# Kernel optimization log

Hardware: AMD Instinct MI355X
Metric: run time of the kernel (lower is better)

Reference implementation:

```python
import jax, jax.numpy as jnp
import numpy as np
import math

B, S, HID = 1, 2048, 4096
NH, NKV, HD = 32, 8, 128
N_REP = NH // NKV
ROPE_THETA = 10000.0


def setup_inputs() -> dict:
    key = jax.random.key(0)
    ks = jax.random.split(key, 5)
    hidden_states = jax.random.normal(ks[0], (B, S, HID), dtype=jnp.float32)
    # additive causal mask: 0 on/below diagonal, -1e9 above
    causal = jnp.triu(jnp.full((S, S), -1e9, dtype=jnp.float32), k=1)
    attention_mask = causal[None, None, :, :]
    wq = jax.random.normal(ks[1], (HID, NH * HD), dtype=jnp.float32) * 0.02
    wk = jax.random.normal(ks[2], (HID, NKV * HD), dtype=jnp.float32) * 0.02
    wv = jax.random.normal(ks[3], (HID, NKV * HD), dtype=jnp.float32) * 0.02
    wo = jax.random.normal(ks[4], (NH * HD, HID), dtype=jnp.float32) * 0.02
    return {"hidden_states": hidden_states, "attention_mask": attention_mask,
            "wq": wq, "wk": wk, "wv": wv, "wo": wo}


def _rope_cos_sin(seq_len, head_dim, base, dtype):
    inv_freq = 1.0 / (base ** (jnp.arange(0, head_dim, 2, dtype=jnp.float32) / head_dim))
    t = jnp.arange(seq_len, dtype=jnp.float32)
    freqs = jnp.outer(t, inv_freq)          # [S, HD/2]
    emb = jnp.concatenate([freqs, freqs], axis=-1)  # [S, HD]
    return jnp.cos(emb).astype(dtype), jnp.sin(emb).astype(dtype)


def _rotate_interleaved(x):
    # pairs (x0,x1) -> (-x1, x0), interleaved (matches torch stack/reshape trick)
    xp = x.reshape(*x.shape[:-1], -1, 2)
    return jnp.stack([-xp[..., 1], xp[..., 0]], axis=-1).reshape(x.shape)


def reference(hidden_states, attention_mask, wq, wk, wv, wo):
    b, s, _ = hidden_states.shape
    q = (hidden_states @ wq).reshape(b, s, NH, HD).transpose(0, 2, 1, 3)   # [B,NH,S,HD]
    k = (hidden_states @ wk).reshape(b, s, NKV, HD).transpose(0, 2, 1, 3)  # [B,NKV,S,HD]
    v = (hidden_states @ wv).reshape(b, s, NKV, HD).transpose(0, 2, 1, 3)

    cos, sin = _rope_cos_sin(s, HD, ROPE_THETA, hidden_states.dtype)
    cos = cos[None, None, :, :]  # broadcast over batch and heads
    sin = sin[None, None, :, :]
    q = q * cos + _rotate_interleaved(q) * sin
    k = k * cos + _rotate_interleaved(k) * sin

    # repeat_kv: [B,NKV,S,HD] -> [B,NH,S,HD]
    k = jnp.repeat(k, N_REP, axis=1)
    v = jnp.repeat(v, N_REP, axis=1)

    scores = jnp.einsum('bhqd,bhkd->bhqk', q, k) / math.sqrt(HD)
    scores = scores + attention_mask
    attn = jax.nn.softmax(scores.astype(jnp.float32), axis=-1).astype(q.dtype)
    out = jnp.einsum('bhqk,bhkd->bhqd', attn, v)          # [B,NH,S,HD]
    out = out.transpose(0, 2, 1, 3).reshape(b, s, NH * HD)
    return out @ wo
```

## Files before the change

kernel.cpp:

```cpp
#include <hip/hip_runtime.h>

#define S_LEN 2048
#define HID 4096
#define NH 32
#define NKV 8
#define HD 128
#define KVW 1024
#define NQKV 6144

typedef _Float16 f16;
typedef _Float16 f16x8 __attribute__((ext_vector_type(8)));
typedef _Float16 f16x4 __attribute__((ext_vector_type(4)));
typedef float f32x4 __attribute__((ext_vector_type(4)));
typedef float f32x16 __attribute__((ext_vector_type(16)));
typedef unsigned int u32;
typedef u32 u32x4 __attribute__((ext_vector_type(4)));

__device__ __forceinline__ void gll16(const void* g, void* lds) {
  __builtin_amdgcn_global_load_lds((const __attribute__((address_space(1))) void*)g,
                                   (__attribute__((address_space(3))) void*)lds, 16, 0, 0);
}

template<int N> __device__ __forceinline__ void vmwait() {
  if constexpr (N == 0) asm volatile("s_waitcnt vmcnt(0)" ::: "memory");
  else if constexpr (N == 2) asm volatile("s_waitcnt vmcnt(2)" ::: "memory");
  else if constexpr (N == 3) asm volatile("s_waitcnt vmcnt(3)" ::: "memory");
  else if constexpr (N == 4) asm volatile("s_waitcnt vmcnt(4)" ::: "memory");
  else if constexpr (N == 5) asm volatile("s_waitcnt vmcnt(5)" ::: "memory");
  else if constexpr (N == 6) asm volatile("s_waitcnt vmcnt(6)" ::: "memory");
  else if constexpr (N == 7) asm volatile("s_waitcnt vmcnt(7)" ::: "memory");
  else if constexpr (N == 8) asm volatile("s_waitcnt vmcnt(8)" ::: "memory");
  else static_assert(N == 0, "add vmcnt case");
}
#define LGKM0 asm volatile("s_waitcnt lgkmcnt(0)" ::: "memory")
#define BAR() __builtin_amdgcn_s_barrier()

__global__ __launch_bounds__(256) void k_prep(
    const float* __restrict__ hs, const float* __restrict__ wq,
    const float* __restrict__ wk, const float* __restrict__ wv,
    const float* __restrict__ wo,
    f16* __restrict__ Hh, f16* __restrict__ Wt, f16* __restrict__ Wot,
    float4* __restrict__ trig)
{
  __shared__ float tile[32][33];
  int bid = blockIdx.x;
  int t = threadIdx.x;
  if (bid >= 40960) {
    int b2 = bid - 40960;
    if (b2 < 4096) {
      size_t i = ((size_t)b2 * 256 + t) * 8;
      float4 a = *(const float4*)(hs + i);
      float4 b = *(const float4*)(hs + i + 4);
      f16x8 o = { (f16)a.x, (f16)a.y, (f16)a.z, (f16)a.w,
                  (f16)b.x, (f16)b.y, (f16)b.z, (f16)b.w };
      *(f16x8*)(Hh + i) = o;
    } else {
      int id = (b2 - 4096) * 256 + t;
      int s = id >> 6, i = id & 63;
      float f0 = powf(10000.f, -(float)((2 * i) & 63) / 64.f);
      float f1 = powf(10000.f, -(float)((2 * i + 1) & 63) / 64.f);
      float a0 = (float)s * f0, a1 = (float)s * f1;
      trig[id] = make_float4(cosf(a0), cosf(a1), sinf(a0), sinf(a1));
    }
    return;
  }
  const float* src; f16* dst; int N; int r;
  if (bid < 16384)      { src = wq; dst = Wt;                          N = 4096; r = bid; }
  else if (bid < 20480) { src = wk; dst = Wt + (size_t)4096 * 4096;    N = 1024; r = bid - 16384; }
  else if (bid < 24576) { src = wv; dst = Wt + (size_t)5120 * 4096;    N = 1024; r = bid - 20480; }
  else                  { src = wo; dst = Wot;                         N = 4096; r = bid - 24576; }
  int tpr = N >> 5;
  int kb = (r / tpr) * 32, nb = (r % tpr) * 32;
  {
    int kl = t >> 3, ng = t & 7;
    float4 v = *(const float4*)(src + (size_t)(kb + kl) * N + nb + ng * 4);
    tile[kl][ng * 4 + 0] = v.x; tile[kl][ng * 4 + 1] = v.y;
    tile[kl][ng * 4 + 2] = v.z; tile[kl][ng * 4 + 3] = v.w;
  }
  __syncthreads();
  {
    int nl = t >> 3, kg = t & 7;
    f16x4 o = { (f16)tile[kg * 4 + 0][nl], (f16)tile[kg * 4 + 1][nl],
                (f16)tile[kg * 4 + 2][nl], (f16)tile[kg * 4 + 3][nl] };
    *(f16x4*)(dst + (size_t)(nb + nl) * HID + kb + kg * 4) = o;
  }
}

extern __shared__ char smem[];

__global__ __launch_bounds__(512, 2) void k_gemm8(
    const f16* __restrict__ A, const f16* __restrict__ Bt,
    f16* __restrict__ Qr, f16* __restrict__ Kr, f16* __restrict__ Vt,
    const float4* __restrict__ trig)
{
  constexpr int BN = 192;
  constexpr int NF = 3;
  constexpr int BCALLS = BN / 64;
  constexpr int BBYTES = BN * 128;
  constexpr int TI = 4 + BCALLS;
  constexpr int W_END = TI, W_MID = TI + 1;
  constexpr int NT = 64;

  const int tid = threadIdx.x, ln = tid & 63, w = tid >> 6;
  const int la = ln & 15, lg = ln >> 4;
  const int wr = w >> 2, wc = w & 3;

  int bx, by;
  {
    int b = blockIdx.y * gridDim.x + blockIdx.x;
    int cx = gridDim.x >> 3;
    int xcd = b & 7, rr = b >> 3;
    bx = xcd * cx + (rr % cx);
    by = rr / cx;
  }
  const int m0 = by * 256, n0 = bx * BN;

  const char* asrcA[2];
#pragma unroll
  for (int c = 0; c < 2; ++c) {
    int row = c * 128 + (tid >> 2);
    int sg = (tid & 3) ^ ((row >> 1) & 3);
    asrcA[c] = (const char*)A + ((size_t)(m0 + row) * HID) * 2 + (size_t)sg * 16;
  }
  const char* bsrcB[BCALLS];
#pragma unroll
  for (int c = 0; c < BCALLS; ++c) {
    int row = c * 64 + (tid >> 3);
    int g = (tid & 7) ^ (row & 7);
    bsrcB[c] = (const char*)Bt + ((size_t)(n0 + row) * HID) * 2 + (size_t)g * 16;
  }
  char* const Bbase = smem + 65536;
  const int d16 = tid * 16;

  auto stA = [&](int t, int h) {
    char* b = smem + (((2 * t + h) & 3) * 16384) + d16;
    size_t off = (size_t)t * 128 + h * 64;
    gll16(asrcA[0] + off, b); gll16(asrcA[1] + off, b + 8192);
  };
  auto stB = [&](int t, int c) {
    char* b = Bbase + (t % 3) * BBYTES + c * 8192 + d16;
    gll16(bsrcB[c] + (size_t)t * 128, b);
  };
  f16x8 af[4], bf[NF];
  auto ldA = [&](int t, int mh, int ks) {
    const char* sb = smem + (((2 * t + ks) & 3) * 16384);
#pragma unroll
    for (int i = 0; i < 4; ++i) {
      int rl = wr * 128 + mh * 64 + i * 16 + la;
      af[i] = *(const f16x8*)(sb + rl * 64 + ((lg ^ ((rl >> 1) & 3)) * 16));
    }
  };
  auto ldB = [&](int t, int ks) {
    const char* sb = Bbase + (t % 3) * BBYTES;
#pragma unroll
    for (int n = 0; n < NF; ++n) {
      int rb = wc * (NF * 16) + n * 16 + la;
      bf[n] = *(const f16x8*)(sb + rb * 128 + (((ks * 4 + lg) ^ (rb & 7)) * 16));
    }
  };

  f32x4 acc[8][NF] = {};

#define MM12(MH)                                                                      \
  __builtin_amdgcn_s_setprio(1);                                                      \
  _Pragma("unroll")                                                                   \
  for (int i = 0; i < 4; ++i)                                                         \
    _Pragma("unroll")                                                                 \
    for (int n = 0; n < NF; ++n)                                                      \
      acc[(MH)*4 + i][n] =                                                            \
        __builtin_amdgcn_mfma_f32_16x16x32_f16(af[i], bf[n], acc[(MH)*4 + i][n], 0, 0, 0); \
  __builtin_amdgcn_s_setprio(0);

  stA(0, 0); stA(0, 1);
  for (int c = 0; c < BCALLS; ++c) stB(0, c);
  stA(1, 0);
  for (int c = 0; c < BCALLS; ++c) stB(1, c);
  vmwait<BCALLS + 2>();
  BAR();

  for (int t = 0; t < NT; ++t) {
    ldA(t, 0, 0); ldB(t, 0);
    if (t + 1 < NT) stA(t + 1, 1);
    BAR(); LGKM0;
    MM12(0);
    BAR();
    ldA(t, 1, 0);
    if (t + 2 < NT) stB(t + 2, 0);
    BAR(); LGKM0;
    MM12(1);
    if (t < NT - 2) vmwait<W_MID>(); else vmwait<0>();
    BAR();
    ldA(t, 0, 1); ldB(t, 1);
    if (t + 2 < NT) { stA(t + 2, 0); stB(t + 2, 1); }
    BAR(); LGKM0;
    MM12(0);
    BAR();
    ldA(t, 1, 1);
    if (t + 2 < NT) stB(t + 2, 2);
    BAR(); LGKM0;
    MM12(1);
    if (t < NT - 2) vmwait<W_END>(); else vmwait<0>();
    BAR();
  }
#undef MM12

#pragma unroll
  for (int mi = 0; mi < 8; ++mi) {
#pragma unroll
    for (int nf = 0; nf < NF; ++nf) {
      f32x4 fr = acc[mi][nf];
      int n = n0 + wc * (NF * 16) + nf * 16 + la;
      int mr = m0 + wr * 128 + mi * 16 + lg * 4;
      if (n < HID + KVW) {
        int d = n & 127;
#pragma unroll
        for (int r = 0; r < 4; ++r) {
          float v = fr[r];
          float p = __shfl_xor(v, 1);
          float4 tc = trig[(size_t)(mr + r) * 64 + (d >> 1)];
          float cv = (d & 1) ? tc.y : tc.x;
          float sv = (d & 1) ? tc.w : tc.z;
          float o = v * cv + ((d & 1) ? p : -p) * sv;
          if (n < HID) Qr[(size_t)(mr + r) * HID + n] = (f16)o;
          else         Kr[(size_t)(mr + r) * KVW + (n - HID)] = (f16)o;
        }
      } else {
        int nv = n - (HID + KVW);
        f16x4 o4 = { (f16)fr[0], (f16)fr[1], (f16)fr[2], (f16)fr[3] };
        *(f16x4*)(Vt + (size_t)nv * S_LEN + mr) = o4;
      }
    }
  }
}

template<int MODE, int MF, int NF, int WM, int WN>
__global__ __launch_bounds__(WM * WN * 64, 2) void k_gemm4(
    const f16* __restrict__ A, const f16* __restrict__ Bt,
    f16* __restrict__ Qr, f16* __restrict__ Kr, f16* __restrict__ Vt,
    const float4* __restrict__ trig, float* __restrict__ Cout)
{
  constexpr int NTHR = WM * WN * 64;
  constexpr int BM = WM * MF * 16;
  constexpr int BN = WN * NF * 16;
  constexpr int ABYTES = BM * 128;
  constexpr int BBYTES = BN * 128;
  constexpr int RPC = NTHR / 8;
  constexpr int ACALLS = BM / RPC;
  constexpr int BCALLS = BN / RPC;
  constexpr int NT = 64;

  const int tid = threadIdx.x, ln = tid & 63, w = tid >> 6;
  const int la = ln & 15, lg = ln >> 4;
  const int wr = w / WN, wc = w % WN;

  int bx, by;
  {
    int b = blockIdx.y * gridDim.x + blockIdx.x;
    int cx = gridDim.x >> 3;
    int xcd = b & 7, rr = b >> 3;
    bx = xcd * cx + (rr % cx);
    by = rr / cx;
  }
  const int m0 = by * BM, n0 = bx * BN;

  const char* asrc[ACALLS];
  const char* bsrc[BCALLS];
  int adst[ACALLS > BCALLS ? ACALLS : BCALLS];
#pragma unroll
  for (int c = 0; c < ACALLS; ++c) {
    int r = c * RPC + (tid >> 3);
    int g = (tid & 7) ^ (r & 7);
    asrc[c] = (const char*)A + ((size_t)(m0 + r) * HID + (size_t)g * 8) * 2;
    adst[c] = c * NTHR * 16 + tid * 16;
  }
#pragma unroll
  for (int c = 0; c < BCALLS; ++c) {
    int r = c * RPC + (tid >> 3);
    int g = (tid & 7) ^ (r & 7);
    bsrc[c] = (const char*)Bt + ((size_t)(n0 + (r >= BN ? r - BN : r)) * HID + (size_t)g * 8) * 2;
  }

  char* const Bbase = smem + 2 * ABYTES;
  f32x4 acc[MF][NF] = {};

#pragma unroll
  for (int c = 0; c < ACALLS; ++c) gll16(asrc[c], smem + adst[c]);
#pragma unroll
  for (int c = 0; c < BCALLS; ++c) gll16(bsrc[c], Bbase + adst[c]);
#pragma unroll
  for (int c = 0; c < BCALLS; ++c) gll16(bsrc[c] + 128, Bbase + 1 * BBYTES + adst[c]);
#pragma unroll
  for (int c = 0; c < BCALLS; ++c) gll16(bsrc[c] + 256, Bbase + 2 * BBYTES + adst[c]);
  vmwait<2 * BCALLS>();
  __builtin_amdgcn_s_barrier();

  for (int t = 0; t < NT; ++t) {
    if (t + 1 < NT) {
      char* sa = smem + ((t + 1) & 1) * ABYTES;
#pragma unroll
      for (int c = 0; c < ACALLS; ++c) gll16(asrc[c] + (size_t)(t + 1) * 128, sa + adst[c]);
    }
    if (t + 3 < NT) {
      char* sb = Bbase + ((t + 3) & 3) * BBYTES;
#pragma unroll
      for (int c = 0; c < BCALLS; ++c) gll16(bsrc[c] + (size_t)(t + 3) * 128, sb + adst[c]);
    }
    const char* sa = smem + (t & 1) * ABYTES;
    const char* sb = Bbase + (t & 3) * BBYTES;
#pragma unroll
    for (int ks = 0; ks < 2; ++ks) {
      f16x8 af[MF], bf[NF];
#pragma unroll
      for (int i = 0; i < MF; ++i) {
        int rl = wr * MF * 16 + i * 16 + la;
        af[i] = *(const f16x8*)(sa + rl * 128 + (((ks * 4 + lg) ^ (rl & 7)) * 16));
      }
#pragma unroll
      for (int n = 0; n < NF; ++n) {
        int rb = wc * NF * 16 + n * 16 + la;
        bf[n] = *(const f16x8*)(sb + rb * 128 + (((ks * 4 + lg) ^ (rb & 7)) * 16));
      }
      __builtin_amdgcn_s_setprio(1);
#pragma unroll
      for (int i = 0; i < MF; ++i)
#pragma unroll
        for (int n = 0; n < NF; ++n)
          acc[i][n] = __builtin_amdgcn_mfma_f32_16x16x32_f16(af[i], bf[n], acc[i][n], 0, 0, 0);
      __builtin_amdgcn_s_setprio(0);
    }
    if (t < NT - 3)      vmwait<BCALLS>();
    else if (t < NT - 1) vmwait<0>();
    if (t < NT - 1) __builtin_amdgcn_s_barrier();
  }

#pragma unroll
  for (int mi = 0; mi < MF; ++mi) {
#pragma unroll
    for (int nf = 0; nf < NF; ++nf) {
      f32x4 fr = acc[mi][nf];
      int n = n0 + wc * NF * 16 + nf * 16 + la;
      int mr = m0 + wr * MF * 16 + mi * 16 + lg * 4;
      if (MODE == 1) {
#pragma unroll
        for (int r = 0; r < 4; ++r)
          Cout[(size_t)(mr + r) * HID + n] = fr[r];
      }
    }
  }
}

#define KBYTES (64 * 128 * 2)
#define VBYTES (128 * 64 * 2)

__global__ __launch_bounds__(256, 2) void k_attn(
    const f16* __restrict__ Qr, const f16* __restrict__ Kr, const f16* __restrict__ Vt,
    f16* __restrict__ AO)
{
  int bid = blockIdx.x;
  int h, c;
  if (bid < 256) { h = bid >> 3; c = bid & 7; }
  else           { int t = bid - 256; h = t >> 3; c = 15 - (t & 7); }
  const int hkv = h >> 2;
  const int q0c = c * 128;
  const int NT = 2 * c + 2;

  __shared__ char KV[2][KBYTES + VBYTES];

  const int tid = threadIdx.x;
  const int ln = tid & 63, w = tid >> 6;
  const int q = ln & 31;
  const int hi = ln >> 5;
  const int qg = q0c + w * 32 + q;

  size_t ksrc[4], vsrc[4];
  int kdo[4], vdo[4];
#pragma unroll
  for (int j = 0; j < 4; ++j) {
    int kc = w * 4 + j;
    int kr = kc * 4 + (ln >> 4);
    ksrc[j] = ((size_t)kr * KVW + hkv * HD) * 2 + (size_t)(((ln & 15) ^ (kr & 7)) * 16);
    kdo[j] = kc * 1024;
    int vc = w * 4 + j;
    int d = vc * 8 + (ln >> 3);
    vsrc[j] = ((size_t)(hkv * HD + d) * S_LEN) * 2 + (size_t)(((ln & 7) ^ (d & 7)) * 16);
    vdo[j] = KBYTES + vc * 1024;
  }

  f16x8 qf[8];
  {
    const f16* qrow = Qr + (size_t)qg * HID + h * HD + hi * 8;
#pragma unroll
    for (int ks = 0; ks < 8; ++ks) qf[ks] = *(const f16x8*)(qrow + ks * 16);
  }

  f32x16 ot[4] = {};
  float m2 = -3.0e38f, l = 0.f;
  const float K2 = 0.12753256471f;

  int buf = 0;
#pragma unroll
  for (int j = 0; j < 4; ++j) {
    gll16((const char*)Kr + ksrc[j], &KV[0][kdo[j]]);
    gll16((const char*)Vt + vsrc[j], &KV[0][vdo[j]]);
  }

  for (int jt = 0; jt < NT; ++jt) {
    __syncthreads();
    if (jt + 1 < NT) {
      size_t ko = (size_t)(jt + 1) * 64 * KVW * 2;
      size_t vo = (size_t)(jt + 1) * 64 * 2;
#pragma unroll
      for (int j = 0; j < 4; ++j) {
        gll16((const char*)Kr + ksrc[j] + ko, &KV[buf ^ 1][kdo[j]]);
        gll16((const char*)Vt + vsrc[j] + vo, &KV[buf ^ 1][vdo[j]]);
      }
    }
    const int j0 = jt * 64;
    if (j0 <= q0c + w * 32 + 31) {
      const f16* Kb = (const f16*)&KV[buf][0];
      const f16* Vb = (const f16*)&KV[buf][KBYTES];
      f32x16 s0 = {}, s1 = {};
#pragma unroll
      for (int ks = 0; ks < 8; ++ks) {
        int cc = ((ks * 2 + hi) ^ (q & 7)) * 8;
        f16x8 k0 = *(const f16x8*)(Kb + q * 128 + cc);
        f16x8 k1 = *(const f16x8*)(Kb + (q + 32) * 128 + cc);
        s0 = __builtin_amdgcn_mfma_f32_32x32x16_f16(k0, qf[ks], s0, 0, 0, 0);
        s1 = __builtin_amdgcn_mfma_f32_32x32x16_f16(k1, qf[ks], s1, 0, 0, 0);
      }
      const bool nm = (j0 + 63 > q0c + w * 32);
      float p0[16], p1[16];
      float mx = -3.0e38f;
#pragma unroll
      for (int r = 0; r < 16; ++r) {
        float a = s0[r], b = s1[r];
        if (nm) {
          int kvb = j0 + (r & 3) + 8 * (r >> 2) + 4 * hi;
          if (kvb > qg) a = -3.0e38f;
          if (kvb + 32 > qg) b = -3.0e38f;
        }
        p0[r] = a; p1[r] = b;
        mx = fmaxf(mx, fmaxf(a, b));
      }
      mx = fmaxf(mx, __shfl_xor(mx, 32));
      float m2c = mx * K2;
      int defer = (m2c <= m2 + 11.0f);
      if (!__all(defer)) {
        float m2n = fmaxf(m2, m2c);
        float corr = exp2f(m2 - m2n);
        m2 = m2n; l *= corr;
#pragma unroll
        for (int t = 0; t < 4; ++t)
#pragma unroll
          for (int r = 0; r < 16; ++r) ot[t][r] *= corr;
      }
      float sum = 0.f;
#pragma unroll
      for (int r = 0; r < 16; ++r) {
        p0[r] = exp2f(__builtin_fmaf(p0[r], K2, -m2));
        p1[r] = exp2f(__builtin_fmaf(p1[r], K2, -m2));
        sum += p0[r] + p1[r];
      }
      l += sum + __shfl_xor(sum, 32);
      u32 pw0[8], pw1[8];
#pragma unroll
      for (int t = 0; t < 8; ++t) {
        pw0[t] = __builtin_bit_cast(u32, __builtin_amdgcn_cvt_pkrtz(p0[2 * t], p0[2 * t + 1]));
        pw1[t] = __builtin_bit_cast(u32, __builtin_amdgcn_cvt_pkrtz(p1[2 * t], p1[2 * t + 1]));
      }
      f16x8 pf[4];
#pragma unroll
      for (int ch = 0; ch < 2; ++ch) {
        const u32* pw = ch ? pw1 : pw0;
        u32 sx[8];
#pragma unroll
        for (int t = 0; t < 8; ++t) sx[t] = (u32)__shfl_xor((int)pw[t], 32);
        u32x4 fa = { hi ? sx[2] : pw[0], hi ? sx[3] : pw[1],
                     hi ? pw[2] : sx[0], hi ? pw[3] : sx[1] };
        u32x4 fb = { hi ? sx[6] : pw[4], hi ? sx[7] : pw[5],
                     hi ? pw[6] : sx[4], hi ? pw[7] : sx[5] };
        pf[ch * 2 + 0] = __builtin_bit_cast(f16x8, fa);
        pf[ch * 2 + 1] = __builtin_bit_cast(f16x8, fb);
      }
#pragma unroll
      for (int dt = 0; dt < 4; ++dt) {
        int d = dt * 32 + q;
#pragma unroll
        for (int f = 0; f < 4; ++f) {
          f16x8 vf = *(const f16x8*)(Vb + d * 64 + (((f * 2 + hi) ^ (q & 7)) * 8));
          ot[dt] = __builtin_amdgcn_mfma_f32_32x32x16_f16(vf, pf[f], ot[dt], 0, 0, 0);
        }
      }
    }
    buf ^= 1;
  }

  __syncthreads();
  char* scr = &KV[0][0] + w * 8192;
  float inv = 1.f / l;
#pragma unroll
  for (int dt = 0; dt < 4; ++dt) {
#pragma unroll
    for (int rg = 0; rg < 4; ++rg) {
      u32 wa = __builtin_bit_cast(u32, __builtin_amdgcn_cvt_pkrtz(ot[dt][rg * 4 + 0] * inv, ot[dt][rg * 4 + 1] * inv));
      u32 wb = __builtin_bit_cast(u32, __builtin_amdgcn_cvt_pkrtz(ot[dt][rg * 4 + 2] * inv, ot[dt][rg * 4 + 3] * inv));
      int byte = q * 256 + (((dt * 4 + rg) ^ (q & 7)) * 16) + hi * 8;
      u32* p = (u32*)(scr + byte);
      p[0] = wa; p[1] = wb;
    }
  }
  asm volatile("s_waitcnt lgkmcnt(0)" ::: "memory");
#pragma unroll
  for (int ps = 0; ps < 8; ++ps) {
    int qr = ps * 4 + (ln >> 4);
    int ck = (ln & 15) ^ (qr & 7);
    f16x8 v = *(const f16x8*)(scr + qr * 256 + ck * 16);
    *(f16x8*)(AO + (size_t)(q0c + w * 32 + qr) * HID + h * HD + (ln & 15) * 8) = v;
  }
}

extern "C" void kernel_launch(void* const* d_in, const int* in_sizes, int n_in,
                              void* d_out, int out_size, void* d_ws, size_t ws_size,
                              hipStream_t stream) {
  const float* hs = (const float*)d_in[0];
  const float* wq = (const float*)d_in[2];
  const float* wk = (const float*)d_in[3];
  const float* wv = (const float*)d_in[4];
  const float* wo = (const float*)d_in[5];
  float* out = (float*)d_out;

  char* ws = (char*)d_ws;
  size_t off = 0;
  auto alloc = [&](size_t b) { char* p = ws + off; off += (b + 255) & ~(size_t)255; return p; };
  f16* Hh   = (f16*)alloc((size_t)S_LEN * HID * 2);
  f16* Wt   = (f16*)alloc((size_t)NQKV * HID * 2);
  float4* trig = (float4*)alloc((size_t)S_LEN * 64 * sizeof(float4));
  f16* Qrp  = (f16*)alloc((size_t)S_LEN * HID * 2);
  f16* Krp  = (f16*)alloc((size_t)S_LEN * KVW * 2);
  f16* Vtp  = (f16*)alloc((size_t)KVW * S_LEN * 2);
  f16* AO   = (f16*)alloc((size_t)S_LEN * HID * 2);
  f16* Wot  = (f16*)alloc((size_t)HID * HID * 2);

  hipFuncSetAttribute((const void*)k_gemm8,
                      hipFuncAttributeMaxDynamicSharedMemorySize, 139264);
  hipFuncSetAttribute((const void*)k_gemm4<1, 8, 2, 2, 4>,
                      hipFuncAttributeMaxDynamicSharedMemorySize, 131072);

  k_prep<<<45568, 256, 0, stream>>>(hs, wq, wk, wv, wo, Hh, Wt, Wot, trig);
  k_gemm8<<<dim3(NQKV / 192, S_LEN / 256), 512, 139264, stream>>>(
      Hh, Wt, Qrp, Krp, Vtp, trig);
  k_attn<<<dim3(512), 256, 0, stream>>>(Qrp, Krp, Vtp, AO);
  k_gemm4<1, 8, 2, 2, 4><<<dim3(HID / 128, S_LEN / 256), 512, 131072, stream>>>(
      AO, Wot, nullptr, nullptr, nullptr, nullptr, out);
}
```

Baseline: 323.4 us.

## Reuse gemm8 pipeline for output projection and widen prep transpose tiles

The output projection GEMM now uses the templated k_gemm8 kernel, with BN=128 and a plain fp32 store epilogue, in place of the separate k_gemm4 kernel. That swaps in the finer-grained A/B staging schedule the QKV GEMM already uses. The weight transpose/convert kernel moves from 32x32 to 64x64 tiles with wider f16x8 stores, cutting block count and store instructions. The risks are different LDS needs (114688 bytes) and that the gemm8 wait counts must still be correct when BCALLS=2.

```diff
diff --git a/kernel.cpp b/kernel.cpp
--- a/kernel.cpp
+++ b/kernel.cpp
@@ -42,11 +42,11 @@
     f16* __restrict__ Hh, f16* __restrict__ Wt, f16* __restrict__ Wot,
     float4* __restrict__ trig)
 {
-  __shared__ float tile[32][33];
+  __shared__ float tile[64][65];
   int bid = blockIdx.x;
   int t = threadIdx.x;
-  if (bid >= 40960) {
-    int b2 = bid - 40960;
+  if (bid >= 10240) {
+    int b2 = bid - 10240;
     if (b2 < 4096) {
       size_t i = ((size_t)b2 * 256 + t) * 8;
       float4 a = *(const float4*)(hs + i);
@@ -65,36 +65,44 @@
     return;
   }
   const float* src; f16* dst; int N; int r;
-  if (bid < 16384)      { src = wq; dst = Wt;                          N = 4096; r = bid; }
-  else if (bid < 20480) { src = wk; dst = Wt + (size_t)4096 * 4096;    N = 1024; r = bid - 16384; }
-  else if (bid < 24576) { src = wv; dst = Wt + (size_t)5120 * 4096;    N = 1024; r = bid - 20480; }
-  else                  { src = wo; dst = Wot;                         N = 4096; r = bid - 24576; }
-  int tpr = N >> 5;
-  int kb = (r / tpr) * 32, nb = (r % tpr) * 32;
+  if (bid < 4096)       { src = wq; dst = Wt;                          N = 4096; r = bid; }
+  else if (bid < 5120)  { src = wk; dst = Wt + (size_t)4096 * 4096;    N = 1024; r = bid - 4096; }
+  else if (bid < 6144)  { src = wv; dst = Wt + (size_t)5120 * 4096;    N = 1024; r = bid - 5120; }
+  else                  { src = wo; dst = Wot;                         N = 4096; r = bid - 6144; }
+  int tpr = N >> 6;
+  int kb = (r / tpr) * 64, nb = (r % tpr) * 64;
   {
-    int kl = t >> 3, ng = t & 7;
-    float4 v = *(const float4*)(src + (size_t)(kb + kl) * N + nb + ng * 4);
-    tile[kl][ng * 4 + 0] = v.x; tile[kl][ng * 4 + 1] = v.y;
-    tile[kl][ng * 4 + 2] = v.z; tile[kl][ng * 4 + 3] = v.w;
+    int kl = t >> 2, c4 = t & 3;
+#pragma unroll
+    for (int i = 0; i < 4; ++i) {
+      float4 v = *(const float4*)(src + (size_t)(kb + kl) * N + nb + c4 * 16 + i * 4);
+      tile[kl][c4 * 16 + i * 4 + 0] = v.x; tile[kl][c4 * 16 + i * 4 + 1] = v.y;
+      tile[kl][c4 * 16 + i * 4 + 2] = v.z; tile[kl][c4 * 16 + i * 4 + 3] = v.w;
+    }
   }
   __syncthreads();
   {
-    int nl = t >> 3, kg = t & 7;
-    f16x4 o = { (f16)tile[kg * 4 + 0][nl], (f16)tile[kg * 4 + 1][nl],
-                (f16)tile[kg * 4 + 2][nl], (f16)tile[kg * 4 + 3][nl] };
-    *(f16x4*)(dst + (size_t)(nb + nl) * HID + kb + kg * 4) = o;
+    int nl = t >> 2, kc = t & 3;
+    f16x8 o0, o1;
+#pragma unroll
+    for (int j = 0; j < 8; ++j) o0[j] = (f16)tile[kc * 16 + j][nl];
+#pragma unroll
+    for (int j = 0; j < 8; ++j) o1[j] = (f16)tile[kc * 16 + 8 + j][nl];
+    f16* dp = dst + (size_t)(nb + nl) * HID + kb + kc * 16;
+    *(f16x8*)dp = o0;
+    *(f16x8*)(dp + 8) = o1;
   }
 }
 
 extern __shared__ char smem[];
 
+template<int MODE, int BN>
 __global__ __launch_bounds__(512, 2) void k_gemm8(
     const f16* __restrict__ A, const f16* __restrict__ Bt,
     f16* __restrict__ Qr, f16* __restrict__ Kr, f16* __restrict__ Vt,
-    const float4* __restrict__ trig)
+    const float4* __restrict__ trig, float* __restrict__ Cout)
 {
-  constexpr int BN = 192;
-  constexpr int NF = 3;
+  constexpr int NF = BN / 64;
   constexpr int BCALLS = BN / 64;
   constexpr int BBYTES = BN * 128;
   constexpr int TI = 4 + BCALLS;
@@ -161,7 +169,7 @@
 
   f32x4 acc[8][NF] = {};
 
-#define MM12(MH)                                                                      \
+#define MMC(MH)                                                                       \
   __builtin_amdgcn_s_setprio(1);                                                      \
   _Pragma("unroll")                                                                   \
   for (int i = 0; i < 4; ++i)                                                         \
@@ -182,27 +190,27 @@
     ldA(t, 0, 0); ldB(t, 0);
     if (t + 1 < NT) stA(t + 1, 1);
     BAR(); LGKM0;
-    MM12(0);
+    MMC(0);
     BAR();
     ldA(t, 1, 0);
     if (t + 2 < NT) stB(t + 2, 0);
     BAR(); LGKM0;
-    MM12(1);
+    MMC(1);
     if (t < NT - 2) vmwait<W_MID>(); else vmwait<0>();
     BAR();
     ldA(t, 0, 1); ldB(t, 1);
-    if (t + 2 < NT) { stA(t + 2, 0); stB(t + 2, 1); }
+    if (t + 2 < NT) { stA(t + 2, 0); if (BCALLS > 1) stB(t + 2, 1); }
     BAR(); LGKM0;
-    MM12(0);
+    MMC(0);
     BAR();
     ldA(t, 1, 1);
-    if (t + 2 < NT) stB(t + 2, 2);
+    if (t + 2 < NT) { if (BCALLS > 2) stB(t + 2, 2); }
     BAR(); LGKM0;
-    MM12(1);
+    MMC(1);
     if (t < NT - 2) vmwait<W_END>(); else vmwait<0>();
     BAR();
   }
-#undef MM12
+#undef MMC
 
 #pragma unroll
   for (int mi = 0; mi < 8; ++mi) {
@@ -211,136 +219,26 @@
       f32x4 fr = acc[mi][nf];
       int n = n0 + wc * (NF * 16) + nf * 16 + la;
       int mr = m0 + wr * 128 + mi * 16 + lg * 4;
-      if (n < HID + KVW) {
-        int d = n & 127;
-#pragma unroll
-        for (int r = 0; r < 4; ++r) {
-          float v = fr[r];
-          float p = __shfl_xor(v, 1);
-          float4 tc = trig[(size_t)(mr + r) * 64 + (d >> 1)];
-          float cv = (d & 1) ? tc.y : tc.x;
-          float sv = (d & 1) ? tc.w : tc.z;
-          float o = v * cv + ((d & 1) ? p : -p) * sv;
-          if (n < HID) Qr[(size_t)(mr + r) * HID + n] = (f16)o;
-          else         Kr[(size_t)(mr + r) * KVW + (n - HID)] = (f16)o;
+      if (MODE == 0) {
+        if (n < HID + KVW) {
+          int d = n & 127;
+#pragma unroll
+          for (int r = 0; r < 4; ++r) {
+            float v = fr[r];
+            float p = __shfl_xor(v, 1);
+            float4 tc = trig[(size_t)(mr + r) * 64 + (d >> 1)];
+            float cv = (d & 1) ? tc.y : tc.x;
+            float sv = (d & 1) ? tc.w : tc.z;
+            float o = v * cv + ((d & 1) ? p : -p) * sv;
+            if (n < HID) Qr[(size_t)(mr + r) * HID + n] = (f16)o;
+            else         Kr[(size_t)(mr + r) * KVW + (n - HID)] = (f16)o;
+          }
+        } else {
+          int nv = n - (HID + KVW);
+          f16x4 o4 = { (f16)fr[0], (f16)fr[1], (f16)fr[2], (f16)fr[3] };
+          *(f16x4*)(Vt + (size_t)nv * S_LEN + mr) = o4;
         }
       } else {
-        int nv = n - (HID + KVW);
-        f16x4 o4 = { (f16)fr[0], (f16)fr[1], (f16)fr[2], (f16)fr[3] };
-        *(f16x4*)(Vt + (size_t)nv * S_LEN + mr) = o4;
-      }
-    }
-  }
-}
-
-template<int MODE, int MF, int NF, int WM, int WN>
-__global__ __launch_bounds__(WM * WN * 64, 2) void k_gemm4(
-    const f16* __restrict__ A, const f16* __restrict__ Bt,
-    f16* __restrict__ Qr, f16* __restrict__ Kr, f16* __restrict__ Vt,
-    const float4* __restrict__ trig, float* __restrict__ Cout)
-{
-  constexpr int NTHR = WM * WN * 64;
-  constexpr int BM = WM * MF * 16;
-  constexpr int BN = WN * NF * 16;
-  constexpr int ABYTES = BM * 128;
-  constexpr int BBYTES = BN * 128;
-  constexpr int RPC = NTHR / 8;
-  constexpr int ACALLS = BM / RPC;
-  constexpr int BCALLS = BN / RPC;
-  constexpr int NT = 64;
-
-  const int tid = threadIdx.x, ln = tid & 63, w = tid >> 6;
-  const int la = ln & 15, lg = ln >> 4;
-  const int wr = w / WN, wc = w % WN;
-
-  int bx, by;
-  {
-    int b = blockIdx.y * gridDim.x + blockIdx.x;
-    int cx = gridDim.x >> 3;
-    int xcd = b & 7, rr = b >> 3;
-    bx = xcd * cx + (rr % cx);
-    by = rr / cx;
-  }
-  const int m0 = by * BM, n0 = bx * BN;
-
-  const char* asrc[ACALLS];
-  const char* bsrc[BCALLS];
-  int adst[ACALLS > BCALLS ? ACALLS : BCALLS];
-#pragma unroll
-  for (int c = 0; c < ACALLS; ++c) {
-    int r = c * RPC + (tid >> 3);
-    int g = (tid & 7) ^ (r & 7);
-    asrc[c] = (const char*)A + ((size_t)(m0 + r) * HID + (size_t)g * 8) * 2;
-    adst[c] = c * NTHR * 16 + tid * 16;
-  }
-#pragma unroll
-  for (int c = 0; c < BCALLS; ++c) {
-    int r = c * RPC + (tid >> 3);
-    int g = (tid & 7) ^ (r & 7);
-    bsrc[c] = (const char*)Bt + ((size_t)(n0 + (r >= BN ? r - BN : r)) * HID + (size_t)g * 8) * 2;
-  }
-
-  char* const Bbase = smem + 2 * ABYTES;
-  f32x4 acc[MF][NF] = {};
-
-#pragma unroll
-  for (int c = 0; c < ACALLS; ++c) gll16(asrc[c], smem + adst[c]);
-#pragma unroll
-  for (int c = 0; c < BCALLS; ++c) gll16(bsrc[c], Bbase + adst[c]);
-#pragma unroll
-  for (int c = 0; c < BCALLS; ++c) gll16(bsrc[c] + 128, Bbase + 1 * BBYTES + adst[c]);
-#pragma unroll
-  for (int c = 0; c < BCALLS; ++c) gll16(bsrc[c] + 256, Bbase + 2 * BBYTES + adst[c]);
-  vmwait<2 * BCALLS>();
-  __builtin_amdgcn_s_barrier();
-
-  for (int t = 0; t < NT; ++t) {
-    if (t + 1 < NT) {
-      char* sa = smem + ((t + 1) & 1) * ABYTES;
-#pragma unroll
-      for (int c = 0; c < ACALLS; ++c) gll16(asrc[c] + (size_t)(t + 1) * 128, sa + adst[c]);
-    }
-    if (t + 3 < NT) {
-      char* sb = Bbase + ((t + 3) & 3) * BBYTES;
-#pragma unroll
-      for (int c = 0; c < BCALLS; ++c) gll16(bsrc[c] + (size_t)(t + 3) * 128, sb + adst[c]);
-    }
-    const char* sa = smem + (t & 1) * ABYTES;
-    const char* sb = Bbase + (t & 3) * BBYTES;
-#pragma unroll
-    for (int ks = 0; ks < 2; ++ks) {
-      f16x8 af[MF], bf[NF];
-#pragma unroll
-      for (int i = 0; i < MF; ++i) {
-        int rl = wr * MF * 16 + i * 16 + la;
-        af[i] = *(const f16x8*)(sa + rl * 128 + (((ks * 4 + lg) ^ (rl & 7)) * 16));
-      }
-#pragma unroll
-      for (int n = 0; n < NF; ++n) {
-        int rb = wc * NF * 16 + n * 16 + la;
-        bf[n] = *(const f16x8*)(sb + rb * 128 + (((ks * 4 + lg) ^ (rb & 7)) * 16));
-      }
-      __builtin_amdgcn_s_setprio(1);
-#pragma unroll
-      for (int i = 0; i < MF; ++i)
-#pragma unroll
-        for (int n = 0; n < NF; ++n)
-          acc[i][n] = __builtin_amdgcn_mfma_f32_16x16x32_f16(af[i], bf[n], acc[i][n], 0, 0, 0);
-      __builtin_amdgcn_s_setprio(0);
-    }
-    if (t < NT - 3)      vmwait<BCALLS>();
-    else if (t < NT - 1) vmwait<0>();
-    if (t < NT - 1) __builtin_amdgcn_s_barrier();
-  }
-
-#pragma unroll
-  for (int mi = 0; mi < MF; ++mi) {
-#pragma unroll
-    for (int nf = 0; nf < NF; ++nf) {
-      f32x4 fr = acc[mi][nf];
-      int n = n0 + wc * NF * 16 + nf * 16 + la;
-      int mr = m0 + wr * MF * 16 + mi * 16 + lg * 4;
-      if (MODE == 1) {
 #pragma unroll
         for (int r = 0; r < 4; ++r)
           Cout[(size_t)(mr + r) * HID + n] = fr[r];
@@ -541,15 +439,15 @@
   f16* AO   = (f16*)alloc((size_t)S_LEN * HID * 2);
   f16* Wot  = (f16*)alloc((size_t)HID * HID * 2);
 
-  hipFuncSetAttribute((const void*)k_gemm8,
+  hipFuncSetAttribute((const void*)k_gemm8<0, 192>,
                       hipFuncAttributeMaxDynamicSharedMemorySize, 139264);
-  hipFuncSetAttribute((const void*)k_gemm4<1, 8, 2, 2, 4>,
-                      hipFuncAttributeMaxDynamicSharedMemorySize, 131072);
-
-  k_prep<<<45568, 256, 0, stream>>>(hs, wq, wk, wv, wo, Hh, Wt, Wot, trig);
-  k_gemm8<<<dim3(NQKV / 192, S_LEN / 256), 512, 139264, stream>>>(
-      Hh, Wt, Qrp, Krp, Vtp, trig);
+  hipFuncSetAttribute((const void*)k_gemm8<1, 128>,
+                      hipFuncAttributeMaxDynamicSharedMemorySize, 114688);
+
+  k_prep<<<14848, 256, 0, stream>>>(hs, wq, wk, wv, wo, Hh, Wt, Wot, trig);
+  k_gemm8<0, 192><<<dim3(NQKV / 192, S_LEN / 256), 512, 139264, stream>>>(
+      Hh, Wt, Qrp, Krp, Vtp, trig, nullptr);
   k_attn<<<dim3(512), 256, 0, stream>>>(Qrp, Krp, Vtp, AO);
-  k_gemm4<1, 8, 2, 2, 4><<<dim3(HID / 128, S_LEN / 256), 512, 131072, stream>>>(
+  k_gemm8<1, 128><<<dim3(HID / 128, S_LEN / 256), 512, 114688, stream>>>(
       AO, Wot, nullptr, nullptr, nullptr, nullptr, out);
 }
```

New measurement: 325.0 us. Within noise of the previous version (+0.5%).
